# Performance work log

Measured on AMD Instinct MI355X. Metric: run time of the kernel, lower is better.

Reference implementation:

```python
import jax, jax.numpy as jnp
import numpy as np

N_CONST = 188
P = 16
HIDDEN = 128
DE = 5
DO = 6
N_TARGETS = 5
BATCH = 32


def _edge_indices(n):
    # receiver/sender pairs in the same order as itertools.product, skipping diagonal
    r, s = np.meshgrid(np.arange(n), np.arange(n), indexing='ij')
    mask = r != s
    return jnp.asarray(r[mask]), jnp.asarray(s[mask])  # each [n*(n-1)]


def _linear_params(key, fan_in, fan_out):
    kw, kb = jax.random.split(key)
    w = jax.random.normal(kw, (fan_in, fan_out), jnp.float32) / np.sqrt(fan_in)
    b = jax.random.normal(kb, (fan_out,), jnp.float32) * 0.01
    return w, b


def setup_inputs() -> dict:
    key = jax.random.key(0)
    ks = jax.random.split(key, 10)
    inp = {"x": jax.random.normal(ks[0], (BATCH, N_CONST, P), jnp.float32)}
    h2 = HIDDEN // 2
    dims = [
        ("fr1", 2 * P, HIDDEN), ("fr2", HIDDEN, h2), ("fr3", h2, DE),
        ("fo1", P + DE, HIDDEN), ("fo2", HIDDEN, h2), ("fo3", h2, DO),
        ("fc1", DO * N_CONST, HIDDEN), ("fc2", HIDDEN, h2), ("fc3", h2, N_TARGETS),
    ]
    for i, (name, fi, fo) in enumerate(dims):
        w, b = _linear_params(ks[i + 1], fi, fo)
        inp[name + "_w"] = w
        inp[name + "_b"] = b
    return inp


def reference(x, fr1_w, fr1_b, fr2_w, fr2_b, fr3_w, fr3_b,
              fo1_w, fo1_b, fo2_w, fo2_b, fo3_w, fo3_b,
              fc1_w, fc1_b, fc2_w, fc2_b, fc3_w, fc3_b):
    B, n, p = x.shape
    recv, send = _edge_indices(n)  # [Nr]
    # gather receiver/sender node features (replaces one-hot matmuls with Rr, Rs)
    e_in = jnp.concatenate([x[:, recv], x[:, send]], axis=-1)  # [B, Nr, 2P]
    h = jax.nn.relu(e_in @ fr1_w + fr1_b)
    h = jax.nn.relu(h @ fr2_w + fr2_b)
    E = jax.nn.relu(h @ fr3_w + fr3_b)  # [B, Nr, De]
    # scatter-add edge effects back to receiver nodes (replaces E @ Rr^T)
    Ebar = jnp.zeros((B, n, E.shape[-1]), x.dtype).at[:, recv].add(E)  # [B, N, De]
    c = jnp.concatenate([x, Ebar], axis=-1)  # [B, N, P+De]
    h = jax.nn.relu(c @ fo1_w + fo1_b)
    h = jax.nn.relu(h @ fo2_w + fo2_b)
    O = jax.nn.relu(h @ fo3_w + fo3_b)  # [B, N, Do]
    h = jax.nn.relu(O.reshape(B, -1) @ fc1_w + fc1_b)
    h = jax.nn.relu(h @ fc2_w + fc2_b)
    return h @ fc3_w + fc3_b  # [B, n_targets]
```

## Files before the change

### kernel.cpp

```cpp
#include <hip/hip_runtime.h>

#define BB   32
#define NN   188
#define PP   16
#define HID  128
#define HH2  64
#define DE   5
#define DO   6
#define NT   5
#define ROWS_O (BB*NN)
#define RT   32
#define KO   (PP+DE)

typedef __attribute__((ext_vector_type(8))) short short8;
typedef __attribute__((ext_vector_type(4))) float float4_;
typedef __attribute__((ext_vector_type(4))) unsigned uint4_;

__device__ __forceinline__ short f2bf(float v) {
    union { float f; unsigned u; } a; a.f = v;
    unsigned r = a.u + 0x7fff + ((a.u >> 16) & 1);
    return (short)(r >> 16);
}
__device__ __forceinline__ unsigned relu_pk(float lo, float hi) {
    float l = lo > 0.f ? lo : 0.f;
    float h = hi > 0.f ? hi : 0.f;
    unsigned r;
    asm("v_cvt_pk_bf16_f32 %0, %1, %2" : "=v"(r) : "v"(l), "v"(h));
    return r;
}

#define XB_OFF    0
#define XB_ELTS   (BB*NN*24)
#define W1T_OFF   (XB_OFF + XB_ELTS)
#define W1T_ELTS  (HID*40)
#define W2S_OFF   (W1T_OFF + W1T_ELTS)
#define W2S_ELTS  (16*64*8)
#define W3S_OFF   (W2S_OFF + W2S_ELTS)
#define W3S_ELTS  (2*64*8)
#define SHORT_TOTAL (W3S_OFF + W3S_ELTS)

__device__ __forceinline__ int kmap(int q, int e) {
    return (e < 4) ? (q*4 + e) : (16 + q*4 + (e - 4));
}

__global__ void prep_kernel(const float* __restrict__ x,
                            const float* __restrict__ w1,
                            const float* __restrict__ w2,
                            const float* __restrict__ w3,
                            short* __restrict__ ws)
{
    const int i = blockIdx.x * blockDim.x + threadIdx.x;
    const int stride = gridDim.x * blockDim.x;
    for (int idx = i; idx < BB*NN*PP; idx += stride) {
        int row = idx >> 4, k = idx & 15;
        ws[XB_OFF + row*24 + k] = f2bf(x[idx]);
    }
    for (int idx = i; idx < 32*HID; idx += stride) {
        int k = idx >> 7, n = idx & 127;
        ws[W1T_OFF + n*40 + k] = f2bf(w1[idx]);
    }
    for (int idx = i; idx < W2S_ELTS; idx += stride) {
        int f = idx >> 9;
        int l = (idx >> 3) & 63;
        int e = idx & 7;
        int tt = f >> 2, s = f & 3;
        int q = l >> 4, n16 = l & 15;
        int k = 32*s + kmap(q, e);
        int n = tt*16 + n16;
        ws[W2S_OFF + idx] = f2bf(w2[k*HH2 + n]);
    }
    for (int idx = i; idx < W3S_ELTS; idx += stride) {
        int s2 = idx >> 9;
        int l = (idx >> 3) & 63;
        int e = idx & 7;
        int q = l >> 4, n16 = l & 15;
        int k = 32*s2 + kmap(q, e);
        ws[W3S_OFF + idx] = (n16 < DE) ? f2bf(w3[k*DE + n16]) : (short)0;
    }
}

__global__ __launch_bounds__(256, 6)
void edge_mfma_kernel(const short* __restrict__ ws_s,
                      const float* __restrict__ b1,
                      const float* __restrict__ b2,
                      const float* __restrict__ b3,
                      float* __restrict__ ebar)
{
    const short* xb  = ws_s + XB_OFF;
    const short* w1t = ws_s + W1T_OFF;
    const short* w3g = ws_s + W3S_OFF;

    __shared__ __align__(16) unsigned wsmem[4096];
    __shared__ __align__(16) short sW1[8*64*8];
    __shared__ __align__(16) float sB1[HID];
    __shared__ __align__(16) float sB2[HH2];

    const int tid  = threadIdx.x;
    const int wave = tid >> 6;
    const int lane = tid & 63;
    const int n16  = lane & 15;
    const int q    = lane >> 4;
    const int bi   = blockIdx.x * 4 + wave;
    const int b    = bi / NN;
    const int recv = bi - b*NN;

    {
        const uint4* src = (const uint4*)(ws_s + W2S_OFF);
        uint4* dst = (uint4*)wsmem;
        #pragma unroll
        for (int i = 0; i < 4; ++i) dst[tid + i*256] = src[tid + i*256];
    }
    #pragma unroll
    for (int i = 0; i < 2; ++i) {
        int f  = tid + i*256;
        int t  = f >> 6, l = f & 63;
        int qq = l >> 4, nn = l & 15;
        uint4 v = *(const uint4*)(w1t + (t*16 + nn)*40 + qq*8);
        *((uint4*)sW1 + f) = v;
    }
    if (tid < HID) sB1[tid] = b1[tid];
    else if (tid < HID + HH2) sB2[tid - HID] = b2[tid - HID];

    short8 W3f[2];
    #pragma unroll
    for (int s = 0; s < 2; ++s)
        W3f[s] = *(const short8*)(w3g + s*512 + lane*8);
    float4_ bias3r;
    #pragma unroll
    for (int rg = 0; rg < 4; ++rg) {
        int o = q*4 + rg;
        bias3r[rg] = (o < DE) ? b3[o] : 0.f;
    }

    __syncthreads();

    const short* w2l = (const short*)wsmem;
    const short8* w1l = (const short8*)sW1;
    const short* xrow = xb + b*(NN*24);
    const bool rside = (q < 2);

    float acc[4] = {0.f, 0.f, 0.f, 0.f};

    short8 E1;
    {
        int send0 = n16 + (n16 >= recv ? 1 : 0);
        const int node = rside ? recv : send0;
        E1 = *(const short8*)(xrow + node*24 + (q & 1)*8);
    }

    #pragma unroll 1
    for (int ti = 0; ti < 12; ++ti) {
        short8 E1c = E1;
        if (ti < 11) {
            int en = (ti+1)*16 + n16;
            int send = en + (en >= recv ? 1 : 0);
            if (send > NN-1) send = NN-1;
            const int node = rside ? recv : send;
            E1 = *(const short8*)(xrow + node*24 + (q & 1)*8);
        }

        float4_ C2[4];
        #pragma unroll
        for (int tt = 0; tt < 4; ++tt)
            C2[tt] = *(const float4_*)(sB2 + tt*16 + q*4);

        #pragma unroll
        for (int s = 0; s < 4; ++s) {
            float4_ cb0 = *(const float4_*)(sB1 + (2*s)*16   + q*4);
            float4_ cb1 = *(const float4_*)(sB1 + (2*s+1)*16 + q*4);
            short8 A1a = w1l[(2*s)*64   + lane];
            short8 A1b = w1l[(2*s+1)*64 + lane];
            float4_ Ca = __builtin_amdgcn_mfma_f32_16x16x32_bf16(A1a, E1c, cb0, 0, 0, 0);
            float4_ Cb = __builtin_amdgcn_mfma_f32_16x16x32_bf16(A1b, E1c, cb1, 0, 0, 0);
            uint4_ dv = (uint4_){ relu_pk(Ca[0], Ca[1]),
                                  relu_pk(Ca[2], Ca[3]),
                                  relu_pk(Cb[0], Cb[1]),
                                  relu_pk(Cb[2], Cb[3]) };
            short8 Bf = __builtin_bit_cast(short8, dv);
            #pragma unroll
            for (int tt = 0; tt < 4; ++tt) {
                short8 A2 = *(const short8*)(w2l + (tt*4 + s)*512 + lane*8);
                C2[tt] = __builtin_amdgcn_mfma_f32_16x16x32_bf16(A2, Bf, C2[tt], 0, 0, 0);
            }
        }

        float4_ C3 = bias3r;
        #pragma unroll
        for (int s2 = 0; s2 < 2; ++s2) {
            float4_ Cc = C2[2*s2], Cd = C2[2*s2+1];
            uint4_ dv = (uint4_){ relu_pk(Cc[0], Cc[1]),
                                  relu_pk(Cc[2], Cc[3]),
                                  relu_pk(Cd[0], Cd[1]),
                                  relu_pk(Cd[2], Cd[3]) };
            short8 B3f = __builtin_bit_cast(short8, dv);
            C3 = __builtin_amdgcn_mfma_f32_16x16x32_bf16(W3f[s2], B3f, C3, 0, 0, 0);
        }
        const int e = ti*16 + n16;
        const bool ok = (e < NN-1);
        #pragma unroll
        for (int rg = 0; rg < 4; ++rg) {
            float v = C3[rg];
            v = v > 0.f ? v : 0.f;
            acc[rg] += ok ? v : 0.f;
        }
    }

    #pragma unroll
    for (int rg = 0; rg < 4; ++rg) {
        acc[rg] += __shfl_xor(acc[rg], 1);
        acc[rg] += __shfl_xor(acc[rg], 2);
        acc[rg] += __shfl_xor(acc[rg], 4);
        acc[rg] += __shfl_xor(acc[rg], 8);
    }
    if (n16 == 0) {
        #pragma unroll
        for (int rg = 0; rg < 4; ++rg) {
            int o = q*4 + rg;
            if (o < DE) ebar[bi*DE + o] = acc[rg];
        }
    }
}

__global__ __launch_bounds__(512)
void obj_mlp_kernel(const float* __restrict__ x, const float* __restrict__ ebar,
                    const float* __restrict__ w1, const float* __restrict__ b1,
                    const float* __restrict__ w2, const float* __restrict__ b2,
                    const float* __restrict__ w3, const float* __restrict__ b3,
                    float* __restrict__ o_out)
{
    __shared__ float sW[HID*HH2];
    __shared__ float sB1[HID];
    __shared__ float sB2[HH2];
    __shared__ float sCin[RT*KO];
    __shared__ float sH1[RT*HID];
    __shared__ float sH2t[HH2*(RT+1)];
    const int tid = threadIdx.x;
    const int rbase = blockIdx.x * RT;

    for (int i = tid; i < KO*HID; i += 512) sW[i] = w1[i];
    if (tid < HID) sB1[tid] = b1[tid];
    else if (tid < HID+HH2) sB2[tid-HID] = b2[tid-HID];
    for (int i = tid; i < RT*KO; i += 512) {
        int r = i / KO, k = i - r*KO;
        int gr = rbase + r;
        int b = gr / NN;
        int node = gr - b*NN;
        sCin[i] = (k < PP) ? x[(b*NN+node)*PP + k]
                           : ebar[(b*NN+node)*DE + (k-PP)];
    }
    __syncthreads();

    {
        const int j = tid & (HID-1);
        const int g = tid >> 7;
        float w[KO];
        #pragma unroll
        for (int k = 0; k < KO; ++k) w[k] = sW[k*HID + j];
        const float bj = sB1[j];
        #pragma unroll
        for (int rr = 0; rr < 8; ++rr) {
            const int r = g*8 + rr;
            const float* e = &sCin[r*KO];
            float a0=0.f,a1=0.f,a2=0.f;
            #pragma unroll
            for (int k = 0; k < KO; k += 3) {
                a0 += w[k+0]*e[k+0];
                a1 += w[k+1]*e[k+1];
                a2 += w[k+2]*e[k+2];
            }
            float v = a0+a1+a2+bj;
            sH1[r*HID + j] = v > 0.f ? v : 0.f;
        }
    }
    __syncthreads();
    for (int i = tid; i < HID*HH2; i += 512) sW[i] = w2[i];
    __syncthreads();

    {
        const int j = tid & (HH2-1);
        const int g = tid >> 6;
        float acc[4];
        #pragma unroll
        for (int rr = 0; rr < 4; ++rr) acc[rr] = sB2[j];
        #pragma unroll
        for (int kc = 0; kc < HID; kc += 32) {
            float w[32];
            #pragma unroll
            for (int kk = 0; kk < 32; ++kk) w[kk] = sW[(kc+kk)*HH2 + j];
            #pragma unroll
            for (int rr = 0; rr < 4; ++rr) {
                const float* h = &sH1[(g*4+rr)*HID + kc];
                float a0=0.f,a1=0.f,a2=0.f,a3=0.f;
                #pragma unroll
                for (int kk = 0; kk < 32; kk += 4) {
                    a0 += w[kk+0]*h[kk+0];
                    a1 += w[kk+1]*h[kk+1];
                    a2 += w[kk+2]*h[kk+2];
                    a3 += w[kk+3]*h[kk+3];
                }
                acc[rr] += (a0+a1)+(a2+a3);
            }
        }
        #pragma unroll
        for (int rr = 0; rr < 4; ++rr) {
            float v = acc[rr];
            sH2t[j*(RT+1) + (g*4+rr)] = v > 0.f ? v : 0.f;
        }
    }
    __syncthreads();

    if (tid < RT*DO) {
        const int r = tid & (RT-1);
        const int c = tid >> 5;
        float a0=0.f,a1=0.f,a2=0.f,a3=0.f;
        #pragma unroll
        for (int k = 0; k < HH2; k += 4) {
            a0 += sH2t[(k+0)*(RT+1)+r]*w3[(k+0)*DO+c];
            a1 += sH2t[(k+1)*(RT+1)+r]*w3[(k+1)*DO+c];
            a2 += sH2t[(k+2)*(RT+1)+r]*w3[(k+2)*DO+c];
            a3 += sH2t[(k+3)*(RT+1)+r]*w3[(k+3)*DO+c];
        }
        float v = (a0+a1)+(a2+a3) + b3[c];
        v = v > 0.f ? v : 0.f;
        int gr = rbase + r;
        int b = gr / NN;
        int node = gr - b*NN;
        o_out[b*(NN*DO) + node*DO + c] = v;
    }
}

__global__ __launch_bounds__(256)
void fc_kernel(const float* __restrict__ o_in,
               const float* __restrict__ w1, const float* __restrict__ b1,
               const float* __restrict__ w2, const float* __restrict__ b2,
               const float* __restrict__ w3, const float* __restrict__ b3,
               float* __restrict__ out)
{
    __shared__ __align__(16) float s_in[NN*DO];
    __shared__ float s_p[256];
    __shared__ float s_h1[HID];
    __shared__ float s_h2[HH2];
    const int b = blockIdx.x, tid = threadIdx.x;

    for (int i = tid; i < NN*DO; i += 256) s_in[i] = o_in[b*(NN*DO) + i];
    __syncthreads();

    {
        const int j = tid & (HID-1);
        const int h = tid >> 7;
        const float4* s4 = (const float4*)&s_in[h*564];
        const float* wbase = w1 + (size_t)(h*564)*HID + j;
        float a0=0.f,a1=0.f,a2=0.f,a3=0.f;
        #pragma unroll 4
        for (int i = 0; i < 141; ++i) {
            float4 v = s4[i];
            const float* wp = wbase + (size_t)i*4*HID;
            a0 += v.x * wp[0];
            a1 += v.y * wp[HID];
            a2 += v.z * wp[2*HID];
            a3 += v.w * wp[3*HID];
        }
        s_p[tid] = (a0+a1)+(a2+a3);
    }
    __syncthreads();
    if (tid < HID) {
        float v = s_p[tid] + s_p[tid+HID] + b1[tid];
        s_h1[tid] = v > 0.f ? v : 0.f;
    }
    __syncthreads();

    {
        const int j = tid & (HH2-1);
        const int q = tid >> 6;
        float acc = 0.f;
        #pragma unroll
        for (int kk = 0; kk < 32; ++kk) {
            int k = q*32 + kk;
            acc += s_h1[k] * w2[k*HH2 + j];
        }
        s_p[tid] = acc;
    }
    __syncthreads();
    if (tid < HH2) {
        float v = s_p[tid] + s_p[tid+64] + s_p[tid+128] + s_p[tid+192] + b2[tid];
        s_h2[tid] = v > 0.f ? v : 0.f;
    }
    __syncthreads();

    if (tid < NT) {
        float acc = b3[tid];
        #pragma unroll
        for (int k = 0; k < HH2; ++k)
            acc += s_h2[k] * w3[k*NT + tid];
        out[b*NT + tid] = acc;
    }
}

extern "C" void kernel_launch(void* const* d_in, const int* in_sizes, int n_in,
                              void* d_out, int out_size, void* d_ws, size_t ws_size,
                              hipStream_t stream) {
    (void)in_sizes; (void)n_in; (void)out_size; (void)ws_size;
    const float* x     = (const float*)d_in[0];
    const float* fr1_w = (const float*)d_in[1];
    const float* fr1_b = (const float*)d_in[2];
    const float* fr2_w = (const float*)d_in[3];
    const float* fr2_b = (const float*)d_in[4];
    const float* fr3_w = (const float*)d_in[5];
    const float* fr3_b = (const float*)d_in[6];
    const float* fo1_w = (const float*)d_in[7];
    const float* fo1_b = (const float*)d_in[8];
    const float* fo2_w = (const float*)d_in[9];
    const float* fo2_b = (const float*)d_in[10];
    const float* fo3_w = (const float*)d_in[11];
    const float* fo3_b = (const float*)d_in[12];
    const float* fc1_w = (const float*)d_in[13];
    const float* fc1_b = (const float*)d_in[14];
    const float* fc2_w = (const float*)d_in[15];
    const float* fc2_b = (const float*)d_in[16];
    const float* fc3_w = (const float*)d_in[17];
    const float* fc3_b = (const float*)d_in[18];

    short* ws_s = (short*)d_ws;
    size_t fbase = ((size_t)SHORT_TOTAL*2 + 15) & ~(size_t)15;
    float* ebar = (float*)((char*)d_ws + fbase);
    float* o_ws = ebar + BB*NN*DE;

    prep_kernel<<<128, 256, 0, stream>>>(x, fr1_w, fr2_w, fr3_w, ws_s);
    edge_mfma_kernel<<<(BB*NN)/4, 256, 0, stream>>>(ws_s, fr1_b, fr2_b, fr3_b, ebar);
    obj_mlp_kernel<<<ROWS_O/RT, 512, 0, stream>>>(
        x, ebar, fo1_w, fo1_b, fo2_w, fo2_b, fo3_w, fo3_b, o_ws);
    fc_kernel<<<BB, 256, 0, stream>>>(
        o_ws, fc1_w, fc1_b, fc2_w, fc2_b, fc3_w, fc3_b, (float*)d_out);
}
```

Baseline: 174.1 us.

## Keep edge-MLP weights and biases in registers instead of LDS

The edge MLP kernel now loads all W1, W2, W3 fragments and the bias vectors straight from global memory into per-lane registers, once per wave, in MFMA-ready layout. Shared memory staging and the block barrier are removed, and the prep kernel writes W1 pre-swizzled into fragment order. This drops the per-iteration LDS reads in the inner MFMA loop. In exchange it needs many more VGPRs, so launch bounds go from 6 to 2 blocks per CU, which lowers occupancy and the ability to hide latency.

```diff
diff --git a/kernel.cpp b/kernel.cpp
--- a/kernel.cpp
+++ b/kernel.cpp
@@ -31,9 +31,9 @@
 
 #define XB_OFF    0
 #define XB_ELTS   (BB*NN*24)
-#define W1T_OFF   (XB_OFF + XB_ELTS)
-#define W1T_ELTS  (HID*40)
-#define W2S_OFF   (W1T_OFF + W1T_ELTS)
+#define W1S_OFF   (XB_OFF + XB_ELTS)
+#define W1S_ELTS  (8*64*8)
+#define W2S_OFF   (W1S_OFF + W1S_ELTS)
 #define W2S_ELTS  (16*64*8)
 #define W3S_OFF   (W2S_OFF + W2S_ELTS)
 #define W3S_ELTS  (2*64*8)
@@ -55,9 +55,12 @@
         int row = idx >> 4, k = idx & 15;
         ws[XB_OFF + row*24 + k] = f2bf(x[idx]);
     }
-    for (int idx = i; idx < 32*HID; idx += stride) {
-        int k = idx >> 7, n = idx & 127;
-        ws[W1T_OFF + n*40 + k] = f2bf(w1[idx]);
+    for (int idx = i; idx < W1S_ELTS; idx += stride) {
+        int t = idx >> 9;
+        int l = (idx >> 3) & 63;
+        int e = idx & 7;
+        int q = l >> 4, n16 = l & 15;
+        ws[W1S_OFF + idx] = f2bf(w1[(q*8 + e)*HID + t*16 + n16]);
     }
     for (int idx = i; idx < W2S_ELTS; idx += stride) {
         int f = idx >> 9;
@@ -79,7 +82,7 @@
     }
 }
 
-__global__ __launch_bounds__(256, 6)
+__global__ __launch_bounds__(256, 2)
 void edge_mfma_kernel(const short* __restrict__ ws_s,
                       const float* __restrict__ b1,
                       const float* __restrict__ b2,
@@ -87,13 +90,9 @@
                       float* __restrict__ ebar)
 {
     const short* xb  = ws_s + XB_OFF;
-    const short* w1t = ws_s + W1T_OFF;
+    const short* w1g = ws_s + W1S_OFF;
+    const short* w2g = ws_s + W2S_OFF;
     const short* w3g = ws_s + W3S_OFF;
-
-    __shared__ __align__(16) unsigned wsmem[4096];
-    __shared__ __align__(16) short sW1[8*64*8];
-    __shared__ __align__(16) float sB1[HID];
-    __shared__ __align__(16) float sB2[HH2];
 
     const int tid  = threadIdx.x;
     const int wave = tid >> 6;
@@ -104,27 +103,26 @@
     const int b    = bi / NN;
     const int recv = bi - b*NN;
 
-    {
-        const uint4* src = (const uint4*)(ws_s + W2S_OFF);
-        uint4* dst = (uint4*)wsmem;
-        #pragma unroll
-        for (int i = 0; i < 4; ++i) dst[tid + i*256] = src[tid + i*256];
-    }
-    #pragma unroll
-    for (int i = 0; i < 2; ++i) {
-        int f  = tid + i*256;
-        int t  = f >> 6, l = f & 63;
-        int qq = l >> 4, nn = l & 15;
-        uint4 v = *(const uint4*)(w1t + (t*16 + nn)*40 + qq*8);
-        *((uint4*)sW1 + f) = v;
-    }
-    if (tid < HID) sB1[tid] = b1[tid];
-    else if (tid < HID + HH2) sB2[tid - HID] = b2[tid - HID];
-
+    short8 W1f[8];
+    #pragma unroll
+    for (int t = 0; t < 8; ++t)
+        W1f[t] = *(const short8*)(w1g + t*512 + lane*8);
+    short8 W2f[16];
+    #pragma unroll
+    for (int f = 0; f < 16; ++f)
+        W2f[f] = *(const short8*)(w2g + f*512 + lane*8);
     short8 W3f[2];
     #pragma unroll
     for (int s = 0; s < 2; ++s)
         W3f[s] = *(const short8*)(w3g + s*512 + lane*8);
+    float4_ cbv[8];
+    #pragma unroll
+    for (int t = 0; t < 8; ++t)
+        cbv[t] = *(const float4_*)(b1 + t*16 + q*4);
+    float4_ bias2v[4];
+    #pragma unroll
+    for (int tt = 0; tt < 4; ++tt)
+        bias2v[tt] = *(const float4_*)(b2 + tt*16 + q*4);
     float4_ bias3r;
     #pragma unroll
     for (int rg = 0; rg < 4; ++rg) {
@@ -132,10 +130,6 @@
         bias3r[rg] = (o < DE) ? b3[o] : 0.f;
     }
 
-    __syncthreads();
-
-    const short* w2l = (const short*)wsmem;
-    const short8* w1l = (const short8*)sW1;
     const short* xrow = xb + b*(NN*24);
     const bool rside = (q < 2);
 
@@ -161,27 +155,20 @@
 
         float4_ C2[4];
         #pragma unroll
-        for (int tt = 0; tt < 4; ++tt)
-            C2[tt] = *(const float4_*)(sB2 + tt*16 + q*4);
+        for (int tt = 0; tt < 4; ++tt) C2[tt] = bias2v[tt];
 
         #pragma unroll
         for (int s = 0; s < 4; ++s) {
-            float4_ cb0 = *(const float4_*)(sB1 + (2*s)*16   + q*4);
-            float4_ cb1 = *(const float4_*)(sB1 + (2*s+1)*16 + q*4);
-            short8 A1a = w1l[(2*s)*64   + lane];
-            short8 A1b = w1l[(2*s+1)*64 + lane];
-            float4_ Ca = __builtin_amdgcn_mfma_f32_16x16x32_bf16(A1a, E1c, cb0, 0, 0, 0);
-            float4_ Cb = __builtin_amdgcn_mfma_f32_16x16x32_bf16(A1b, E1c, cb1, 0, 0, 0);
+            float4_ Ca = __builtin_amdgcn_mfma_f32_16x16x32_bf16(W1f[2*s],   E1c, cbv[2*s],   0, 0, 0);
+            float4_ Cb = __builtin_amdgcn_mfma_f32_16x16x32_bf16(W1f[2*s+1], E1c, cbv[2*s+1], 0, 0, 0);
             uint4_ dv = (uint4_){ relu_pk(Ca[0], Ca[1]),
                                   relu_pk(Ca[2], Ca[3]),
                                   relu_pk(Cb[0], Cb[1]),
                                   relu_pk(Cb[2], Cb[3]) };
             short8 Bf = __builtin_bit_cast(short8, dv);
             #pragma unroll
-            for (int tt = 0; tt < 4; ++tt) {
-                short8 A2 = *(const short8*)(w2l + (tt*4 + s)*512 + lane*8);
-                C2[tt] = __builtin_amdgcn_mfma_f32_16x16x32_bf16(A2, Bf, C2[tt], 0, 0, 0);
-            }
+            for (int tt = 0; tt < 4; ++tt)
+                C2[tt] = __builtin_amdgcn_mfma_f32_16x16x32_bf16(W2f[tt*4 + s], Bf, C2[tt], 0, 0, 0);
         }
 
         float4_ C3 = bias3r;
```

Result: faster. 163.4 us (-6.1%).
